# Optimization experiments

Hardware: AMD Instinct MI355X
Metric: run time of the kernel (lower is better)

## Reference

```python
import jax, jax.numpy as jnp
import numpy as np

B, E = 256, 512
C, K = 8192, 10          # n_class, n_center
LMD = 10.0
INV_GAMMA = 10.0         # 1 / gamma, gamma = 0.1
TAU = 0.2
MARGIN = 0.01


def setup_inputs() -> dict:
    key = jax.random.key(0)
    k1, k2, k3 = jax.random.split(key, 3)
    embeddings = jax.random.normal(k1, (B, E), dtype=jnp.float32)
    labels = jax.random.randint(k2, (B,), 0, C, dtype=jnp.int64)
    fc = jax.random.normal(k3, (C * K, E), dtype=jnp.float32)
    return {"embeddings": embeddings, "labels": labels, "fc": fc}


def reference(embeddings, labels, fc):
    # L2-normalize centers (rows of fc), like F.normalize(fc, p=2, dim=1)
    norm = jnp.sqrt(jnp.sum(fc * fc, axis=1, keepdims=True))
    w = fc / jnp.maximum(norm, 1e-12)

    # similarity to every center: [B, C, K]
    x = (embeddings @ w.T).reshape(B, C, K)
    prob = jax.nn.softmax(INV_GAMMA * x, axis=2)
    h = jnp.sum(prob * x, axis=2)  # [B, C] soft-pooled class similarity

    # subtract margin on ground-truth class, then cross-entropy
    rows = jnp.arange(B)
    margin_m = jnp.zeros_like(h).at[rows, labels].set(MARGIN)
    logits = LMD * (h - margin_m)
    logp = jax.nn.log_softmax(logits, axis=1)
    loss_cls = -jnp.mean(logp[rows, labels])

    # regularizer: batched per-class center gram, replaces python loop over C
    wc = w.reshape(C, K, E)
    sub = 1.0 - jnp.einsum('cke,cje->ckj', wc, wc)   # [C, K, K]
    sub = jnp.where(sub <= 0.0, 1e-10, sub)
    mask = jnp.triu(jnp.ones((K, K), dtype=bool), k=1)  # strict upper triangle
    safe = jnp.where(mask, 2.0 * sub, 1.0)
    reg = jnp.sum(jnp.where(mask, jnp.sqrt(safe), 0.0))
    reg = reg / (C * K * (K - 1.0))
    return loss_cls + TAU * reg
```

## Files before the change

kernel.cpp:

```cpp
#include <hip/hip_runtime.h>


typedef __bf16 bf16;
typedef bf16 bf16x8 __attribute__((ext_vector_type(8)));
typedef float f32x4 __attribute__((ext_vector_type(4)));

#define NCLASS 8192
#define KC 10
#define EDIM 512
#define BATCH 256
#define BK 64

__device__ inline void load_lds16(const void* g, void* l) {
    __builtin_amdgcn_global_load_lds(
        (const __attribute__((address_space(1))) void*)g,
        (__attribute__((address_space(3))) void*)l, 16, 0, 0);
}

__global__ __launch_bounds__(256) void prep_kernel(
    const float* __restrict__ fc, bf16* __restrict__ w,
    float* __restrict__ gram_part,
    const float* __restrict__ e, bf16* __restrict__ At,
    float* __restrict__ sumexp)
{
    const int t = threadIdx.x;

    if (blockIdx.x >= 2048) {
        if (blockIdx.x == 2048 + 64) {
            sumexp[t] = 0.0f;
            return;
        }
        int i = (blockIdx.x - 2048) * 256 + t;
        int row = i >> 6, chunk = i & 63;
        int k = chunk * 8;
        float4 a = ((const float4*)e)[i * 2];
        float4 b = ((const float4*)e)[i * 2 + 1];
        bf16x8 v;
        v[0] = (bf16)a.x; v[1] = (bf16)a.y; v[2] = (bf16)a.z; v[3] = (bf16)a.w;
        v[4] = (bf16)b.x; v[5] = (bf16)b.y; v[6] = (bf16)b.z; v[7] = (bf16)b.w;
        *(bf16x8*)&At[((k >> 5) << 13) + (row << 5) + (k & 31)] = v;
        return;
    }

    const int wave = t >> 6, lane = t & 63;
    const int c = blockIdx.x * 4 + wave;

    float4 ra[KC][2];
    #pragma unroll
    for (int r = 0; r < KC; ++r) {
        const float4* rp =
            (const float4*)(fc + ((size_t)c * KC + r) * EDIM) + lane * 2;
        ra[r][0] = rp[0];
        ra[r][1] = rp[1];
    }

    float invn[KC];
    #pragma unroll
    for (int r = 0; r < KC; ++r) {
        float4 a = ra[r][0], b = ra[r][1];
        float s = a.x*a.x + a.y*a.y + a.z*a.z + a.w*a.w
                + b.x*b.x + b.y*b.y + b.z*b.z + b.w*b.w;
        #pragma unroll
        for (int off = 32; off; off >>= 1) s += __shfl_xor(s, off);
        invn[r] = 1.0f / fmaxf(sqrtf(s), 1e-12f);
    }

    float part = 0.f;
    #pragma unroll
    for (int i = 0; i < KC - 1; ++i) {
        #pragma unroll
        for (int j = i + 1; j < KC; ++j) {
            float4 ai = ra[i][0], bi = ra[i][1];
            float4 aj = ra[j][0], bj = ra[j][1];
            float s = ai.x*aj.x + ai.y*aj.y + ai.z*aj.z + ai.w*aj.w
                    + bi.x*bj.x + bi.y*bj.y + bi.z*bj.z + bi.w*bj.w;
            #pragma unroll
            for (int off = 32; off; off >>= 1) s += __shfl_xor(s, off);
            float sub = 1.0f - s * invn[i] * invn[j];
            if (sub <= 0.0f) sub = 1e-10f;
            part += sqrtf(2.0f * sub);
        }
    }
    if (lane == 0) gram_part[c] = part;

    #pragma unroll
    for (int r = 0; r < KC; ++r) {
        float inv = invn[r];
        float4 a = ra[r][0], b = ra[r][1];
        bf16x8 v;
        v[0] = (bf16)(a.x * inv); v[1] = (bf16)(a.y * inv);
        v[2] = (bf16)(a.z * inv); v[3] = (bf16)(a.w * inv);
        v[4] = (bf16)(b.x * inv); v[5] = (bf16)(b.y * inv);
        v[6] = (bf16)(b.z * inv); v[7] = (bf16)(b.w * inv);
        *(bf16x8*)&w[((size_t)c * KC + r) * EDIM + lane * 8] = v;
    }
}

__global__ __launch_bounds__(512, 2) void gemm_h_kernel(
    const bf16* __restrict__ W,
    const bf16* __restrict__ At,
    const int* __restrict__ labels,
    float* __restrict__ sumexp,
    float* __restrict__ lab_logit)
{
    __shared__ bf16 Ws[2][80 * BK];
    const int tid = threadIdx.x;
    const int wave = tid >> 6, lane = tid & 63;

    f32x4 acc[5][2];
    #pragma unroll
    for (int mt = 0; mt < 5; ++mt)
        #pragma unroll
        for (int nt = 0; nt < 2; ++nt)
            acc[mt][nt] = (f32x4){0.f, 0.f, 0.f, 0.f};

    const size_t g0 = (size_t)blockIdx.x * 80;

    const int rA = tid >> 3, sA = tid & 7;
    const bf16* srcA = W + (g0 + rA) * EDIM + ((sA ^ (rA & 7)) << 3);
    const int rB = (512 + tid) >> 3, sB = tid & 7;
    const bf16* srcB = W + (g0 + rB) * EDIM + ((sB ^ (rB & 7)) << 3);

    const int q = lane >> 4;
    const int q8 = q * 8;
    const int fr = lane & 15;

    load_lds16(srcA, &Ws[0][wave * 512]);
    if (tid < 128) load_lds16(srcB, &Ws[0][4096 + wave * 512]);
    __syncthreads();

    for (int t = 0; t < 8; ++t) {
        const int cur = t & 1;
        if (t < 7) {
            const int kb = (t + 1) * BK;
            load_lds16(srcA + kb, &Ws[cur ^ 1][wave * 512]);
            if (tid < 128) load_lds16(srcB + kb, &Ws[cur ^ 1][4096 + wave * 512]);
        }
        #pragma unroll
        for (int kk = 0; kk < BK; kk += 32) {
            const int ccb = kk >> 3;
            bf16x8 wf[5], ef[2];
            #pragma unroll
            for (int nt = 0; nt < 2; ++nt) {
                int row = wave * 32 + nt * 16 + fr;
                ef[nt] = *(const bf16x8*)
                    &At[((t * 2 + (kk >> 5)) << 13) + (row << 5) + q8];
            }
            #pragma unroll
            for (int mt = 0; mt < 5; ++mt) {
                int row = mt * 16 + fr;
                int s = (ccb + q) ^ (row & 7);
                wf[mt] = *(const bf16x8*)&Ws[cur][row * BK + (s << 3)];
            }
            #pragma unroll
            for (int mt = 0; mt < 5; ++mt)
                #pragma unroll
                for (int nt = 0; nt < 2; ++nt)
                    acc[mt][nt] = __builtin_amdgcn_mfma_f32_16x16x32_bf16(
                        wf[mt], ef[nt], acc[mt][nt], 0, 0, 0);
        }
        __syncthreads();
    }

    const int col = lane & 15;
    const int quad = lane >> 4;
    const int cb = blockIdx.x * 8;
    #pragma unroll
    for (int nt = 0; nt < 2; ++nt) {
        int b = wave * 32 + nt * 16 + col;
        float hval[8];
        #pragma unroll
        for (int cc = 0; cc < 8; ++cc) {
            float xm = -1e30f;
            #pragma unroll
            for (int mt = 0; mt < 5; ++mt) {
                if (10 * cc + 10 > 16 * mt && 10 * cc < 16 * mt + 16) {
                    #pragma unroll
                    for (int rg = 0; rg < 4; ++rg) {
                        int r = 16 * mt + 4 * quad + rg;
                        if (r >= 10 * cc && r < 10 * cc + 10)
                            xm = fmaxf(xm, acc[mt][nt][rg]);
                    }
                }
            }
            xm = fmaxf(xm, __shfl_xor(xm, 16));
            xm = fmaxf(xm, __shfl_xor(xm, 32));
            float s1 = 0.f, s2 = 0.f;
            #pragma unroll
            for (int mt = 0; mt < 5; ++mt) {
                if (10 * cc + 10 > 16 * mt && 10 * cc < 16 * mt + 16) {
                    #pragma unroll
                    for (int rg = 0; rg < 4; ++rg) {
                        int r = 16 * mt + 4 * quad + rg;
                        if (r >= 10 * cc && r < 10 * cc + 10) {
                            float x = acc[mt][nt][rg];
                            float e = __expf(10.0f * (x - xm));
                            s1 += e; s2 += e * x;
                        }
                    }
                }
            }
            s1 += __shfl_xor(s1, 16); s1 += __shfl_xor(s1, 32);
            s2 += __shfl_xor(s2, 16); s2 += __shfl_xor(s2, 32);
            hval[cc] = s2 / s1;
        }
        if (quad == 0) {
            const int lbl = labels[b];
            float ps = 0.f;
            #pragma unroll
            for (int cc = 0; cc < 8; ++cc) {
                float lg = 10.0f * hval[cc];
                if (lbl == cb + cc) {
                    lg -= 0.1f;
                    lab_logit[b] = lg;
                }
                ps += __expf(lg);
            }
            atomicAdd(&sumexp[b], ps);
        }
    }
}

__global__ __launch_bounds__(256) void final_kernel(
    const float* __restrict__ gram_part, const float* __restrict__ sumexp,
    const float* __restrict__ lab_logit, float* __restrict__ out)
{
    __shared__ float red[4];
    const int t = threadIdx.x, wave = t >> 6, lane = t & 63;
    const float4* gp4 = (const float4*)gram_part;
    float g = 0.f;
    #pragma unroll
    for (int i = 0; i < 8; ++i) {
        float4 x = gp4[t + i * 256];
        g += x.x + x.y + x.z + x.w;
    }
    float ce = logf(sumexp[t]) - lab_logit[t];
    float val = ce * (1.0f / 256.0f)
              + g * (0.2f / 737280.0f);
    #pragma unroll
    for (int off = 32; off; off >>= 1) val += __shfl_xor(val, off);
    if (lane == 0) red[wave] = val;
    __syncthreads();
    if (t == 0) out[0] = red[0] + red[1] + red[2] + red[3];
}

extern "C" void kernel_launch(void* const* d_in, const int* in_sizes, int n_in,
                              void* d_out, int out_size, void* d_ws, size_t ws_size,
                              hipStream_t stream) {
    const float* emb    = (const float*)d_in[0];
    const int*   labels = (const int*)d_in[1];
    const float* fc     = (const float*)d_in[2];
    float* out = (float*)d_out;

    char* ws = (char*)d_ws;
    bf16*  w         = (bf16*)ws;
    bf16*  At        = (bf16*)(ws + 83886080);
    float* gram_part = (float*)(ws + 84148224);
    float* sumexp    = (float*)(ws + 84181248);
    float* lab_logit = (float*)(ws + 84182272);

    prep_kernel<<<2048 + 65, 256, 0, stream>>>(fc, w, gram_part, emb, At,
                                               sumexp);
    gemm_h_kernel<<<81920 / 80, 512, 0, stream>>>(w, At, labels,
                                                  sumexp, lab_logit);
    final_kernel<<<1, 256, 0, stream>>>(gram_part, sumexp, lab_logit, out);
}
```

Baseline: 309.4 us.

## Fuse fc normalization and center gram into GEMM, reading fp32 fc directly

Removes the separate prep pass that normalized fc into a bf16 copy. The GEMM kernel now loads fp32 fc directly, converts it to bf16 into LDS, and computes per-row norms and the per-class gram through an extra MFMA on the same tile. Normalization is applied afterward to the accumulators. This avoids writing and rereading an 80MB bf16 weight copy, but loses async LDS loads. Norms and gram are now computed from bf16 values instead of fp32, which costs accuracy.

```diff
diff --git a/kernel.cpp b/kernel.cpp
--- a/kernel.cpp
+++ b/kernel.cpp
@@ -11,97 +11,34 @@
 #define BATCH 256
 #define BK 64
 
-__device__ inline void load_lds16(const void* g, void* l) {
-    __builtin_amdgcn_global_load_lds(
-        (const __attribute__((address_space(1))) void*)g,
-        (__attribute__((address_space(3))) void*)l, 16, 0, 0);
-}
-
-__global__ __launch_bounds__(256) void prep_kernel(
-    const float* __restrict__ fc, bf16* __restrict__ w,
-    float* __restrict__ gram_part,
+__global__ __launch_bounds__(256) void conv_kernel(
     const float* __restrict__ e, bf16* __restrict__ At,
-    float* __restrict__ sumexp)
+    float* __restrict__ sumexp, float* __restrict__ gram_sum)
 {
     const int t = threadIdx.x;
-
-    if (blockIdx.x >= 2048) {
-        if (blockIdx.x == 2048 + 64) {
-            sumexp[t] = 0.0f;
-            return;
-        }
-        int i = (blockIdx.x - 2048) * 256 + t;
-        int row = i >> 6, chunk = i & 63;
-        int k = chunk * 8;
-        float4 a = ((const float4*)e)[i * 2];
-        float4 b = ((const float4*)e)[i * 2 + 1];
-        bf16x8 v;
-        v[0] = (bf16)a.x; v[1] = (bf16)a.y; v[2] = (bf16)a.z; v[3] = (bf16)a.w;
-        v[4] = (bf16)b.x; v[5] = (bf16)b.y; v[6] = (bf16)b.z; v[7] = (bf16)b.w;
-        *(bf16x8*)&At[((k >> 5) << 13) + (row << 5) + (k & 31)] = v;
+    if (blockIdx.x == 64) {
+        sumexp[t] = 0.0f;
+        if (t == 0) gram_sum[0] = 0.0f;
         return;
     }
-
-    const int wave = t >> 6, lane = t & 63;
-    const int c = blockIdx.x * 4 + wave;
-
-    float4 ra[KC][2];
-    #pragma unroll
-    for (int r = 0; r < KC; ++r) {
-        const float4* rp =
-            (const float4*)(fc + ((size_t)c * KC + r) * EDIM) + lane * 2;
-        ra[r][0] = rp[0];
-        ra[r][1] = rp[1];
-    }
-
-    float invn[KC];
-    #pragma unroll
-    for (int r = 0; r < KC; ++r) {
-        float4 a = ra[r][0], b = ra[r][1];
-        float s = a.x*a.x + a.y*a.y + a.z*a.z + a.w*a.w
-                + b.x*b.x + b.y*b.y + b.z*b.z + b.w*b.w;
-        #pragma unroll
-        for (int off = 32; off; off >>= 1) s += __shfl_xor(s, off);
-        invn[r] = 1.0f / fmaxf(sqrtf(s), 1e-12f);
-    }
-
-    float part = 0.f;
-    #pragma unroll
-    for (int i = 0; i < KC - 1; ++i) {
-        #pragma unroll
-        for (int j = i + 1; j < KC; ++j) {
-            float4 ai = ra[i][0], bi = ra[i][1];
-            float4 aj = ra[j][0], bj = ra[j][1];
-            float s = ai.x*aj.x + ai.y*aj.y + ai.z*aj.z + ai.w*aj.w
-                    + bi.x*bj.x + bi.y*bj.y + bi.z*bj.z + bi.w*bj.w;
-            #pragma unroll
-            for (int off = 32; off; off >>= 1) s += __shfl_xor(s, off);
-            float sub = 1.0f - s * invn[i] * invn[j];
-            if (sub <= 0.0f) sub = 1e-10f;
-            part += sqrtf(2.0f * sub);
-        }
-    }
-    if (lane == 0) gram_part[c] = part;
-
-    #pragma unroll
-    for (int r = 0; r < KC; ++r) {
-        float inv = invn[r];
-        float4 a = ra[r][0], b = ra[r][1];
-        bf16x8 v;
-        v[0] = (bf16)(a.x * inv); v[1] = (bf16)(a.y * inv);
-        v[2] = (bf16)(a.z * inv); v[3] = (bf16)(a.w * inv);
-        v[4] = (bf16)(b.x * inv); v[5] = (bf16)(b.y * inv);
-        v[6] = (bf16)(b.z * inv); v[7] = (bf16)(b.w * inv);
-        *(bf16x8*)&w[((size_t)c * KC + r) * EDIM + lane * 8] = v;
-    }
-}
-
-__global__ __launch_bounds__(512, 2) void gemm_h_kernel(
-    const bf16* __restrict__ W,
+    int i = blockIdx.x * 256 + t;
+    int row = i >> 6, chunk = i & 63;
+    int k = chunk * 8;
+    float4 a = ((const float4*)e)[i * 2];
+    float4 b = ((const float4*)e)[i * 2 + 1];
+    bf16x8 v;
+    v[0] = (bf16)a.x; v[1] = (bf16)a.y; v[2] = (bf16)a.z; v[3] = (bf16)a.w;
+    v[4] = (bf16)b.x; v[5] = (bf16)b.y; v[6] = (bf16)b.z; v[7] = (bf16)b.w;
+    *(bf16x8*)&At[((k >> 5) << 13) + (row << 5) + (k & 31)] = v;
+}
+
+__global__ __launch_bounds__(512, 2) void gemm_all_kernel(
+    const float* __restrict__ fc,
     const bf16* __restrict__ At,
     const int* __restrict__ labels,
     float* __restrict__ sumexp,
-    float* __restrict__ lab_logit)
+    float* __restrict__ lab_logit,
+    float* __restrict__ gram_sum)
 {
     __shared__ bf16 Ws[2][80 * BK];
     const int tid = threadIdx.x;
@@ -113,33 +50,57 @@
         #pragma unroll
         for (int nt = 0; nt < 2; ++nt)
             acc[mt][nt] = (f32x4){0.f, 0.f, 0.f, 0.f};
+    f32x4 gacc = (f32x4){0.f, 0.f, 0.f, 0.f};
 
     const size_t g0 = (size_t)blockIdx.x * 80;
 
-    const int rA = tid >> 3, sA = tid & 7;
-    const bf16* srcA = W + (g0 + rA) * EDIM + ((sA ^ (rA & 7)) << 3);
-    const int rB = (512 + tid) >> 3, sB = tid & 7;
-    const bf16* srcB = W + (g0 + rB) * EDIM + ((sB ^ (rB & 7)) << 3);
+    const int rowA = tid >> 3, sA = tid & 7;
+    const float* srcA = fc + (g0 + rowA) * EDIM + ((sA ^ (rowA & 7)) << 3);
+    const int rowB = (512 + tid) >> 3, sB = tid & 7;
+    const float* srcB = fc + (g0 + rowB) * EDIM + ((sB ^ (rowB & 7)) << 3);
+    const bool hasB = (tid < 128);
+    const int ldsA = rowA * BK + sA * 8;
+    const int ldsB = rowB * BK + sB * 8;
 
     const int q = lane >> 4;
     const int q8 = q * 8;
     const int fr = lane & 15;
-
-    load_lds16(srcA, &Ws[0][wave * 512]);
-    if (tid < 128) load_lds16(srcB, &Ws[0][4096 + wave * 512]);
+    const int grow = min(10 * wave + fr, 79);
+
+    {
+        float4 a0 = ((const float4*)srcA)[0];
+        float4 a1 = ((const float4*)srcA)[1];
+        bf16x8 va;
+        va[0]=(bf16)a0.x; va[1]=(bf16)a0.y; va[2]=(bf16)a0.z; va[3]=(bf16)a0.w;
+        va[4]=(bf16)a1.x; va[5]=(bf16)a1.y; va[6]=(bf16)a1.z; va[7]=(bf16)a1.w;
+        *(bf16x8*)&Ws[0][ldsA] = va;
+        if (hasB) {
+            float4 b0 = ((const float4*)srcB)[0];
+            float4 b1 = ((const float4*)srcB)[1];
+            bf16x8 vb;
+            vb[0]=(bf16)b0.x; vb[1]=(bf16)b0.y; vb[2]=(bf16)b0.z; vb[3]=(bf16)b0.w;
+            vb[4]=(bf16)b1.x; vb[5]=(bf16)b1.y; vb[6]=(bf16)b1.z; vb[7]=(bf16)b1.w;
+            *(bf16x8*)&Ws[0][ldsB] = vb;
+        }
+    }
     __syncthreads();
 
     for (int t = 0; t < 8; ++t) {
         const int cur = t & 1;
+        float4 a0, a1, b0, b1;
         if (t < 7) {
-            const int kb = (t + 1) * BK;
-            load_lds16(srcA + kb, &Ws[cur ^ 1][wave * 512]);
-            if (tid < 128) load_lds16(srcB + kb, &Ws[cur ^ 1][4096 + wave * 512]);
+            const int k0 = (t + 1) * BK;
+            a0 = ((const float4*)(srcA + k0))[0];
+            a1 = ((const float4*)(srcA + k0))[1];
+            if (hasB) {
+                b0 = ((const float4*)(srcB + k0))[0];
+                b1 = ((const float4*)(srcB + k0))[1];
+            }
         }
         #pragma unroll
         for (int kk = 0; kk < BK; kk += 32) {
             const int ccb = kk >> 3;
-            bf16x8 wf[5], ef[2];
+            bf16x8 wf[5], ef[2], wg;
             #pragma unroll
             for (int nt = 0; nt < 2; ++nt) {
                 int row = wave * 32 + nt * 16 + fr;
@@ -151,6 +112,10 @@
                 int row = mt * 16 + fr;
                 int s = (ccb + q) ^ (row & 7);
                 wf[mt] = *(const bf16x8*)&Ws[cur][row * BK + (s << 3)];
+            }
+            {
+                int s = (ccb + q) ^ (grow & 7);
+                wg = *(const bf16x8*)&Ws[cur][grow * BK + (s << 3)];
             }
             #pragma unroll
             for (int mt = 0; mt < 5; ++mt)
@@ -158,12 +123,69 @@
                 for (int nt = 0; nt < 2; ++nt)
                     acc[mt][nt] = __builtin_amdgcn_mfma_f32_16x16x32_bf16(
                         wf[mt], ef[nt], acc[mt][nt], 0, 0, 0);
+            gacc = __builtin_amdgcn_mfma_f32_16x16x32_bf16(wg, wg, gacc, 0, 0, 0);
+        }
+        if (t < 7) {
+            bf16x8 va;
+            va[0]=(bf16)a0.x; va[1]=(bf16)a0.y; va[2]=(bf16)a0.z; va[3]=(bf16)a0.w;
+            va[4]=(bf16)a1.x; va[5]=(bf16)a1.y; va[6]=(bf16)a1.z; va[7]=(bf16)a1.w;
+            *(bf16x8*)&Ws[cur ^ 1][ldsA] = va;
+            if (hasB) {
+                bf16x8 vb;
+                vb[0]=(bf16)b0.x; vb[1]=(bf16)b0.y; vb[2]=(bf16)b0.z; vb[3]=(bf16)b0.w;
+                vb[4]=(bf16)b1.x; vb[5]=(bf16)b1.y; vb[6]=(bf16)b1.z; vb[7]=(bf16)b1.w;
+                *(bf16x8*)&Ws[cur ^ 1][ldsB] = vb;
+            }
         }
         __syncthreads();
     }
 
+    float* fbuf = (float*)&Ws[0][0];
     const int col = lane & 15;
     const int quad = lane >> 4;
+    #pragma unroll
+    for (int rg = 0; rg < 4; ++rg) {
+        if ((col >> 2) == quad && (col & 3) == rg) {
+            int pr = 10 * wave + col;
+            if (pr < 80) fbuf[pr] = gacc[rg];
+        }
+    }
+    __syncthreads();
+    if (tid < 80) fbuf[80 + tid] = 1.0f / fmaxf(sqrtf(fbuf[tid]), 1e-12f);
+    __syncthreads();
+    const float* invn = fbuf + 80;
+
+    float part = 0.f;
+    #pragma unroll
+    for (int rg = 0; rg < 4; ++rg) {
+        int rr = 4 * quad + rg;
+        if (rr < col && col < 10) {
+            float s_cos = gacc[rg] * invn[10 * wave + rr] * invn[10 * wave + col];
+            float sub = 1.0f - s_cos;
+            if (sub <= 0.0f) sub = 1e-10f;
+            part += sqrtf(2.0f * sub);
+        }
+    }
+    #pragma unroll
+    for (int off = 32; off; off >>= 1) part += __shfl_xor(part, off);
+    if (lane == 0) fbuf[160 + wave] = part;
+    __syncthreads();
+    if (tid == 0) {
+        float g = 0.f;
+        #pragma unroll
+        for (int wv = 0; wv < 8; ++wv) g += fbuf[160 + wv];
+        atomicAdd(gram_sum, g);
+    }
+
+    #pragma unroll
+    for (int mt = 0; mt < 5; ++mt)
+        #pragma unroll
+        for (int rg = 0; rg < 4; ++rg) {
+            float iv = invn[16 * mt + 4 * quad + rg];
+            acc[mt][0][rg] *= iv;
+            acc[mt][1][rg] *= iv;
+        }
+
     const int cb = blockIdx.x * 8;
     #pragma unroll
     for (int nt = 0; nt < 2; ++nt) {
@@ -222,26 +244,19 @@
 }
 
 __global__ __launch_bounds__(256) void final_kernel(
-    const float* __restrict__ gram_part, const float* __restrict__ sumexp,
-    const float* __restrict__ lab_logit, float* __restrict__ out)
+    const float* __restrict__ sumexp, const float* __restrict__ lab_logit,
+    const float* __restrict__ gram_sum, float* __restrict__ out)
 {
     __shared__ float red[4];
     const int t = threadIdx.x, wave = t >> 6, lane = t & 63;
-    const float4* gp4 = (const float4*)gram_part;
-    float g = 0.f;
-    #pragma unroll
-    for (int i = 0; i < 8; ++i) {
-        float4 x = gp4[t + i * 256];
-        g += x.x + x.y + x.z + x.w;
-    }
-    float ce = logf(sumexp[t]) - lab_logit[t];
-    float val = ce * (1.0f / 256.0f)
-              + g * (0.2f / 737280.0f);
+    float val = (logf(sumexp[t]) - lab_logit[t]) * (1.0f / 256.0f);
     #pragma unroll
     for (int off = 32; off; off >>= 1) val += __shfl_xor(val, off);
     if (lane == 0) red[wave] = val;
     __syncthreads();
-    if (t == 0) out[0] = red[0] + red[1] + red[2] + red[3];
+    if (t == 0)
+        out[0] = red[0] + red[1] + red[2] + red[3]
+               + gram_sum[0] * (0.2f / 737280.0f);
 }
 
 extern "C" void kernel_launch(void* const* d_in, const int* in_sizes, int n_in,
@@ -253,15 +268,13 @@
     float* out = (float*)d_out;
 
     char* ws = (char*)d_ws;
-    bf16*  w         = (bf16*)ws;
-    bf16*  At        = (bf16*)(ws + 83886080);
-    float* gram_part = (float*)(ws + 84148224);
-    float* sumexp    = (float*)(ws + 84181248);
-    float* lab_logit = (float*)(ws + 84182272);
-
-    prep_kernel<<<2048 + 65, 256, 0, stream>>>(fc, w, gram_part, emb, At,
-                                               sumexp);
-    gemm_h_kernel<<<81920 / 80, 512, 0, stream>>>(w, At, labels,
-                                                  sumexp, lab_logit);
-    final_kernel<<<1, 256, 0, stream>>>(gram_part, sumexp, lab_logit, out);
-}
+    bf16*  At        = (bf16*)ws;
+    float* sumexp    = (float*)(ws + 262144);
+    float* lab_logit = (float*)(ws + 263168);
+    float* gram_sum  = (float*)(ws + 264192);
+
+    conv_kernel<<<65, 256, 0, stream>>>(emb, At, sumexp, gram_sum);
+    gemm_all_kernel<<<NCLASS / 8, 512, 0, stream>>>(fc, At, labels,
+                                                    sumexp, lab_logit, gram_sum);
+    final_kernel<<<1, 256, 0, stream>>>(sumexp, lab_logit, gram_sum, out);
+}
```

After: 267.0 us. 13.7% less time.
